# Optimization experiments

Hardware: AMD Instinct MI355X
Metric: run time of the kernel (lower is better)

## Reference

```python
import jax, jax.numpy as jnp
import numpy as np

H = 16  # num_heads


def _rotate_half(t):
    d = t.shape[-1] // 2
    return jnp.concatenate((-t[..., d:], t[..., :d]), axis=-1)


def setup_inputs() -> dict:
    key = jax.random.key(0)
    ks = jax.random.split(key, 4)
    S, HID = 2048, 1280
    D = HID // H  # 80
    x = jax.random.normal(ks[0], (S, HID), dtype=jnp.float32)
    # rotary tables (seq_len, head_dim)
    inv_freq = 1.0 / (10000.0 ** (jnp.arange(0, D, 2, dtype=jnp.float32) / D))
    freqs = jnp.arange(S, dtype=jnp.float32)[:, None] * inv_freq[None, :]  # (S, D/2)
    emb = jnp.concatenate([freqs, freqs], axis=-1)  # (S, D)
    cos = jnp.cos(emb)
    sin = jnp.sin(emb)
    W_qkv = jax.random.normal(ks[1], (HID, 3 * HID), dtype=jnp.float32) * 0.02
    b_qkv = jnp.zeros((3 * HID,), dtype=jnp.float32)
    W_out = jax.random.normal(ks[2], (HID, HID), dtype=jnp.float32) * 0.02
    b_out = jnp.zeros((HID,), dtype=jnp.float32)
    # 8 windows of 256 tokens each -> block-diagonal attention
    cu_seqlens = jnp.arange(0, S + 1, 256, dtype=jnp.int32)  # (9,)
    return {"x": x, "cos": cos, "sin": sin, "W_qkv": W_qkv, "b_qkv": b_qkv,
            "W_out": W_out, "b_out": b_out, "cu_seqlens": cu_seqlens}


def _segment_mask(cu_seqlens, seq_len, dtype):
    positions = jnp.arange(seq_len)
    starts = cu_seqlens[:-1]
    ends = cu_seqlens[1:]
    in_segment = (positions[:, None] >= starts[None, :]) & (positions[:, None] < ends[None, :])
    segment_ids = jnp.argmax(in_segment.astype(jnp.int32), axis=-1)  # (S,)
    same_segment = segment_ids[:, None] == segment_ids[None, :]      # (S, S)
    return jnp.where(same_segment, jnp.zeros((), dtype), jnp.finfo(dtype).min)


def reference(x, cos, sin, W_qkv, b_qkv, W_out, b_out, cu_seqlens):
    S, HID = x.shape
    D = HID // H
    scale = D ** -0.5
    qkv = x @ W_qkv + b_qkv                       # (S, 3*HID)
    q, k, v = jnp.split(qkv, 3, axis=-1)
    q = q.reshape(S, H, D)
    k = k.reshape(S, H, D)
    v = v.reshape(S, H, D)
    cos_f = cos[:, :D][:, None, :]                # (S, 1, D)
    sin_f = sin[:, :D][:, None, :]
    q = q * cos_f + _rotate_half(q) * sin_f       # inline RoPE (fp32)
    k = k * cos_f + _rotate_half(k) * sin_f
    q = jnp.transpose(q, (1, 0, 2))               # (H, S, D)
    k = jnp.transpose(k, (1, 0, 2))
    v = jnp.transpose(v, (1, 0, 2))
    scores = jnp.einsum('hqd,hkd->hqk', q, k) * scale  # (H, S, S)
    mask = _segment_mask(cu_seqlens, S, scores.dtype)  # (S, S) block-diagonal bias
    scores = scores + mask[None, :, :]
    weights = jax.nn.softmax(scores, axis=-1)
    out = jnp.einsum('hqk,hkd->hqd', weights, v)       # (H, S, D)
    out = jnp.transpose(out, (1, 0, 2)).reshape(S, HID)
    return out @ W_out + b_out
```

## Files before the change

kernel.cpp:

```cpp
#include <hip/hip_runtime.h>


typedef short s16x8 __attribute__((ext_vector_type(8)));
typedef __bf16 bf16x8 __attribute__((ext_vector_type(8)));
typedef float f32x4 __attribute__((ext_vector_type(4)));
typedef unsigned short u16;
typedef unsigned long long u64;

__device__ __forceinline__ f32x4 mfma16(s16x8 a, s16x8 b, f32x4 c) {
  return __builtin_amdgcn_mfma_f32_16x16x32_bf16(
      __builtin_bit_cast(bf16x8, a), __builtin_bit_cast(bf16x8, b), c, 0, 0, 0);
}
__device__ __forceinline__ u16 f2b(float f) {
  union { float f; unsigned u; } v;
  v.f = f;
  unsigned r = v.u + 0x7fffu + ((v.u >> 16) & 1u);
  return (u16)(r >> 16);
}
__device__ __forceinline__ void gl16(const u16* g, u16* l) {
  __builtin_amdgcn_global_load_lds(
      (const __attribute__((address_space(1))) unsigned int*)(const void*)g,
      (__attribute__((address_space(3))) unsigned int*)(void*)l, 16, 0, 0);
}

__device__ __forceinline__ void transpose_body(const float* __restrict__ W,
                                               u16* __restrict__ WT, int K, int N,
                                               int nb, int kb, int t, float (*tile)[33]) {
  int tx = t & 31, ty = t >> 5;
#pragma unroll
  for (int r = 0; r < 32; r += 8)
    tile[ty + r][tx] = W[(long)(kb + ty + r) * N + nb + tx];
  __syncthreads();
#pragma unroll
  for (int r = 0; r < 32; r += 8)
    WT[(long)(nb + ty + r) * K + kb + tx] = f2b(tile[tx][ty + r]);
}

__global__ __launch_bounds__(256) void prep(const float* __restrict__ x,
                                            u16* __restrict__ xb,
                                            const float* __restrict__ Wqkv,
                                            u16* __restrict__ WqkvT,
                                            const float* __restrict__ Wout,
                                            u16* __restrict__ WoutT) {
  __shared__ float tile[32][33];
  int bid = blockIdx.x, t = threadIdx.x;
  if (bid < 2560) {
    int i = bid * 256 + t;
    float4 v = ((const float4*)x)[i];
    u64 pk = (u64)f2b(v.x) | ((u64)f2b(v.y) << 16) | ((u64)f2b(v.z) << 32) |
             ((u64)f2b(v.w) << 48);
    ((u64*)xb)[i] = pk;
  } else if (bid < 7360) {
    int i = bid - 2560;
    transpose_body(Wqkv, WqkvT, 1280, 3840, (i % 120) * 32, (i / 120) * 32, t, tile);
  } else {
    int i = bid - 7360;
    transpose_body(Wout, WoutT, 1280, 1280, (i % 40) * 32, (i / 40) * 32, t, tile);
  }
}

__global__ __launch_bounds__(512, 4) void gemm_qkv_rope(const u16* __restrict__ A,
                                                        const u16* __restrict__ B,
                                                        const float* __restrict__ bias,
                                                        const float* __restrict__ cosb,
                                                        const float* __restrict__ sinb,
                                                        u16* __restrict__ Qr,
                                                        u16* __restrict__ Kr,
                                                        u16* __restrict__ VT) {
  __shared__ u16 As[2][128 * 64];
  __shared__ u16 Bs[2][160 * 64];
  const int K = 1280;
  int i = blockIdx.x;
  int xcd = i & 7, j = i >> 3;
  int n0 = (xcd * 3 + (j % 3)) * 160;
  int m0 = (j / 3) * 128;
  int t = threadIdx.x, w = t >> 6, lane = t & 63, lm = lane & 15, quad = lane >> 4;
  int wm = (w >> 1) * 32, wn = (w & 1) * 80;

  const u16* AgSrc[2];
  const u16* BgSrc[3];
#pragma unroll
  for (int c = 0; c < 2; c++) {
    int g = c * 512 + t, row = g >> 3, chp = g & 7;
    AgSrc[c] = A + (long)(m0 + row) * K + ((chp ^ (row & 7)) << 3);
  }
#pragma unroll
  for (int c = 0; c < 2; c++) {
    int g = c * 512 + t, row = g >> 3, chp = g & 7;
    BgSrc[c] = B + (long)(n0 + row) * K + ((chp ^ (row & 7)) << 3);
  }
  {
    int g = 1024 + t, row = g >> 3, chp = g & 7;
    BgSrc[2] = B + (long)(n0 + row) * K + ((chp ^ (row & 7)) << 3);
  }

  auto stage = [&](int buf, int k0) {
#pragma unroll
    for (int c = 0; c < 2; c++) gl16(AgSrc[c] + k0, &As[buf][c * 4096 + w * 512]);
#pragma unroll
    for (int c = 0; c < 2; c++) gl16(BgSrc[c] + k0, &Bs[buf][c * 4096 + w * 512]);
    if (t < 256) gl16(BgSrc[2] + k0, &Bs[buf][8192 + w * 512]);
  };

  f32x4 acc[2][5] = {};
  stage(0, 0);
  int buf = 0;
  for (int k0 = 0; k0 < K; k0 += 64) {
    __syncthreads();
    if (k0 + 64 < K) stage(buf ^ 1, k0 + 64);
#pragma unroll
    for (int kh = 0; kh < 2; kh++) {
      s16x8 af[2], bfr[5];
#pragma unroll
      for (int mt = 0; mt < 2; mt++) {
        int rm = wm + mt * 16 + lm;
        af[mt] = *(const s16x8*)&As[buf][rm * 64 + (((kh * 4 + quad) ^ (rm & 7)) << 3)];
      }
#pragma unroll
      for (int nt = 0; nt < 5; nt++) {
        int rn = wn + nt * 16 + lm;
        bfr[nt] = *(const s16x8*)&Bs[buf][rn * 64 + (((kh * 4 + quad) ^ (rn & 7)) << 3)];
      }
#pragma unroll
      for (int mt = 0; mt < 2; mt++)
#pragma unroll
        for (int nt = 0; nt < 5; nt++)
          acc[mt][nt] = mfma16(af[mt], bfr[nt], acc[mt][nt]);
    }
    buf ^= 1;
  }

  int region = n0 / 1280;
  int hcol = (n0 - region * 1280 + wn) / 80;
  float bv[5];
#pragma unroll
  for (int nt = 0; nt < 5; nt++) bv[nt] = bias[n0 + wn + nt * 16 + lm];

  if (region == 2) {
#pragma unroll
    for (int mt = 0; mt < 2; mt++) {
      int sbase = m0 + wm + mt * 16 + quad * 4;
#pragma unroll
      for (int nt = 0; nt < 5; nt++) {
        int d = nt * 16 + lm;
        u64 pk = 0;
#pragma unroll
        for (int r = 0; r < 4; r++)
          pk |= (u64)f2b(acc[mt][nt][r] + bv[nt]) << (16 * r);
        *(u64*)&VT[((long)hcol * 80 + d) * 2048 + sbase] = pk;
      }
    }
    return;
  }

  const float scale = 0.111803398874989f;
  bool lo = lm < 8;
  u16* Out = (region == 0) ? Qr : Kr;
  float oscale = (region == 0) ? scale : 1.0f;
#pragma unroll
  for (int mt = 0; mt < 2; mt++)
#pragma unroll
    for (int r = 0; r < 4; r++) {
      int s = m0 + wm + mt * 16 + quad * 4 + r;
      float val[5], sw[5];
#pragma unroll
      for (int nt = 0; nt < 5; nt++) val[nt] = acc[mt][nt][r] + bv[nt];
#pragma unroll
      for (int nt = 0; nt < 5; nt++) sw[nt] = __shfl_xor(val[nt], 8);
      float rot[5];
      rot[0] = -(lo ? sw[2] : sw[3]);
      rot[1] = -(lo ? sw[3] : sw[4]);
      rot[2] = lo ? -sw[4] : sw[0];
      rot[3] = lo ? sw[0] : sw[1];
      rot[4] = lo ? sw[1] : sw[2];
      u16* orow = Out + ((long)hcol * 2048 + s) * 80;
      const float* crow = cosb + s * 80;
      const float* srw = sinb + s * 80;
#pragma unroll
      for (int nt = 0; nt < 5; nt++) {
        int d = nt * 16 + lm;
        orow[d] = f2b((val[nt] * crow[d] + rot[nt] * srw[d]) * oscale);
      }
    }
}

__global__ __launch_bounds__(512, 2) void gemm_out(const u16* __restrict__ A,
                                                   const u16* __restrict__ B,
                                                   const float* __restrict__ bias,
                                                   float* __restrict__ C) {
  __shared__ u16 As[2][64 * 64];
  __shared__ u16 Bs[2][160 * 64];
  const int K = 1280;
  int i = blockIdx.x;
  int xcd = i & 7, m0 = (i >> 3) * 64, n0 = xcd * 160;
  int t = threadIdx.x, w = t >> 6, lane = t & 63, lm = lane & 15, quad = lane >> 4;
  int wm = (w >> 1) * 16, wn = (w & 1) * 80;

  const u16* AgSrc;
  {
    int row = t >> 3, chp = t & 7;
    AgSrc = A + (long)(m0 + row) * K + ((chp ^ (row & 7)) << 3);
  }
  const u16* BgSrc[3];
#pragma unroll
  for (int c = 0; c < 2; c++) {
    int g = c * 512 + t, row = g >> 3, chp = g & 7;
    BgSrc[c] = B + (long)(n0 + row) * K + ((chp ^ (row & 7)) << 3);
  }
  {
    int g = 1024 + t, row = g >> 3, chp = g & 7;
    BgSrc[2] = B + (long)(n0 + row) * K + ((chp ^ (row & 7)) << 3);
  }

  auto stage = [&](int buf, int k0) {
    gl16(AgSrc + k0, &As[buf][w * 512]);
#pragma unroll
    for (int c = 0; c < 2; c++) gl16(BgSrc[c] + k0, &Bs[buf][c * 4096 + w * 512]);
    if (t < 256) gl16(BgSrc[2] + k0, &Bs[buf][8192 + w * 512]);
  };

  f32x4 acc[5] = {};
  stage(0, 0);
  int buf = 0;
  for (int k0 = 0; k0 < K; k0 += 64) {
    __syncthreads();
    if (k0 + 64 < K) stage(buf ^ 1, k0 + 64);
#pragma unroll
    for (int kh = 0; kh < 2; kh++) {
      int rm = wm + lm;
      s16x8 af = *(const s16x8*)&As[buf][rm * 64 + (((kh * 4 + quad) ^ (rm & 7)) << 3)];
      s16x8 bfr[5];
#pragma unroll
      for (int nt = 0; nt < 5; nt++) {
        int rn = wn + nt * 16 + lm;
        bfr[nt] = *(const s16x8*)&Bs[buf][rn * 64 + (((kh * 4 + quad) ^ (rn & 7)) << 3)];
      }
#pragma unroll
      for (int nt = 0; nt < 5; nt++) acc[nt] = mfma16(af, bfr[nt], acc[nt]);
    }
    buf ^= 1;
  }
#pragma unroll
  for (int nt = 0; nt < 5; nt++) {
    int col = n0 + wn + nt * 16 + lm;
    float bvv = bias[col];
#pragma unroll
    for (int r = 0; r < 4; r++) {
      int row = m0 + wm + quad * 4 + r;
      C[(long)row * 1280 + col] = acc[nt][r] + bvv;
    }
  }
}

__global__ __launch_bounds__(256, 2) void attn_kernel(const u16* __restrict__ Qr,
                                                      const u16* __restrict__ Kr,
                                                      const u16* __restrict__ VT,
                                                      u16* __restrict__ AO) {
  int qb = blockIdx.x, seg = blockIdx.y, h = blockIdx.z;
  int t = threadIdx.x;
  int w = t >> 6, lane = t & 63, lm = lane & 15, quad = lane >> 4;
  __shared__ u16 Ps[4][16 * 256];

  int s0 = seg * 256 + qb * 64 + w * 16;
  const u16* Qh = Qr + ((long)h * 2048 + s0) * 80;
  const u16* Kh = Kr + ((long)h * 2048 + seg * 256) * 80;

  f32x4 sc[16] = {};
  s16x8 zz = {};
#pragma unroll
  for (int kk = 0; kk < 3; kk++) {
    int dbase = kk * 32 + quad * 8;
    bool valid = dbase < 80;
    s16x8 af = valid ? *(const s16x8*)(Qh + lm * 80 + dbase) : zz;
#pragma unroll
    for (int nt = 0; nt < 16; nt++) {
      s16x8 bfr = valid ? *(const s16x8*)(Kh + (nt * 16 + lm) * 80 + dbase) : zz;
      sc[nt] = mfma16(af, bfr, sc[nt]);
    }
  }

  float rowinv[4];
#pragma unroll
  for (int r = 0; r < 4; r++) {
    float m = sc[0][r];
#pragma unroll
    for (int nt = 1; nt < 16; nt++) m = fmaxf(m, sc[nt][r]);
    m = fmaxf(m, __shfl_xor(m, 1));
    m = fmaxf(m, __shfl_xor(m, 2));
    m = fmaxf(m, __shfl_xor(m, 4));
    m = fmaxf(m, __shfl_xor(m, 8));
    float s = 0.f;
#pragma unroll
    for (int nt = 0; nt < 16; nt++) {
      float e = __expf(sc[nt][r] - m);
      sc[nt][r] = e;
      s += e;
    }
    s += __shfl_xor(s, 1);
    s += __shfl_xor(s, 2);
    s += __shfl_xor(s, 4);
    s += __shfl_xor(s, 8);
    rowinv[r] = 1.0f / s;
    int row = quad * 4 + r;
#pragma unroll
    for (int nt = 0; nt < 16; nt++) {
      int chunk = nt * 2 + (lm >> 3);
      Ps[w][row * 256 + ((chunk ^ row) << 3) + (lm & 7)] = f2b(sc[nt][r]);
    }
  }
  asm volatile("s_waitcnt lgkmcnt(0)" ::: "memory");

  f32x4 oacc[5] = {};
  const u16* Vh = VT + (long)h * 80 * 2048 + seg * 256;
#pragma unroll
  for (int kc = 0; kc < 8; kc++) {
    int row = lm;
    s16x8 pa = *(const s16x8*)&Ps[w][row * 256 + (((kc * 4 + quad) ^ row) << 3)];
#pragma unroll
    for (int nt = 0; nt < 5; nt++) {
      s16x8 bvv = *(const s16x8*)(Vh + (long)(nt * 16 + lm) * 2048 + kc * 32 + quad * 8);
      oacc[nt] = mfma16(pa, bvv, oacc[nt]);
    }
  }
#pragma unroll
  for (int nt = 0; nt < 5; nt++)
#pragma unroll
    for (int r = 0; r < 4; r++)
      AO[(long)(s0 + quad * 4 + r) * 1280 + h * 80 + nt * 16 + lm] =
          f2b(oacc[nt][r] * rowinv[r]);
}

extern "C" void kernel_launch(void* const* d_in, const int* in_sizes, int n_in,
                              void* d_out, int out_size, void* d_ws, size_t ws_size,
                              hipStream_t stream) {
  const float* x    = (const float*)d_in[0];
  const float* cosb = (const float*)d_in[1];
  const float* sinb = (const float*)d_in[2];
  const float* Wqkv = (const float*)d_in[3];
  const float* bqkv = (const float*)d_in[4];
  const float* Wout = (const float*)d_in[5];
  const float* bout = (const float*)d_in[6];

  char* p = (char*)d_ws;
  u16* xb    = (u16*)p;
  u16* WqkvT = (u16*)(p + 5242880);
  u16* WoutT = (u16*)(p + 15073280);
  u16* Qr    = (u16*)(p + 18350080);
  u16* Kr    = (u16*)(p + 23592960);
  u16* VT    = (u16*)(p + 28835840);
  u16* AO    = xb;

  prep<<<dim3(8960), dim3(256), 0, stream>>>(x, xb, Wqkv, WqkvT, Wout, WoutT);
  gemm_qkv_rope<<<dim3(384), dim3(512), 0, stream>>>(xb, WqkvT, bqkv, cosb, sinb,
                                                     Qr, Kr, VT);
  attn_kernel<<<dim3(4, 8, 16), dim3(256), 0, stream>>>(Qr, Kr, VT, AO);
  gemm_out<<<dim3(256), dim3(512), 0, stream>>>(AO, WoutT, bout, (float*)d_out);
}
```

Baseline: 161.8 us.

## Fuse prep, QKV GEMM, attention and output GEMM into one cooperative persistent kernel

```diff
diff --git a/kernel.cpp b/kernel.cpp
--- a/kernel.cpp
+++ b/kernel.cpp
@@ -23,6 +23,19 @@
       (__attribute__((address_space(3))) unsigned int*)(void*)l, 16, 0, 0);
 }
 
+__device__ __forceinline__ void grid_barrier(unsigned* bar, unsigned target) {
+  __threadfence();
+  __syncthreads();
+  if (threadIdx.x == 0) {
+    __hip_atomic_fetch_add(bar, 1u, __ATOMIC_RELEASE, __HIP_MEMORY_SCOPE_AGENT);
+    while (__hip_atomic_load(bar, __ATOMIC_ACQUIRE, __HIP_MEMORY_SCOPE_AGENT) <
+           target)
+      __builtin_amdgcn_s_sleep(8);
+  }
+  __syncthreads();
+  __threadfence();
+}
+
 __device__ __forceinline__ void transpose_body(const float* __restrict__ W,
                                                u16* __restrict__ WT, int K, int N,
                                                int nb, int kb, int t, float (*tile)[33]) {
@@ -36,189 +49,273 @@
     WT[(long)(nb + ty + r) * K + kb + tx] = f2b(tile[tx][ty + r]);
 }
 
-__global__ __launch_bounds__(256) void prep(const float* __restrict__ x,
-                                            u16* __restrict__ xb,
-                                            const float* __restrict__ Wqkv,
-                                            u16* __restrict__ WqkvT,
-                                            const float* __restrict__ Wout,
-                                            u16* __restrict__ WoutT) {
-  __shared__ float tile[32][33];
-  int bid = blockIdx.x, t = threadIdx.x;
-  if (bid < 2560) {
-    int i = bid * 256 + t;
-    float4 v = ((const float4*)x)[i];
-    u64 pk = (u64)f2b(v.x) | ((u64)f2b(v.y) << 16) | ((u64)f2b(v.z) << 32) |
-             ((u64)f2b(v.w) << 48);
-    ((u64*)xb)[i] = pk;
-  } else if (bid < 7360) {
-    int i = bid - 2560;
-    transpose_body(Wqkv, WqkvT, 1280, 3840, (i % 120) * 32, (i / 120) * 32, t, tile);
-  } else {
-    int i = bid - 7360;
-    transpose_body(Wout, WoutT, 1280, 1280, (i % 40) * 32, (i / 40) * 32, t, tile);
-  }
-}
-
-__global__ __launch_bounds__(512, 4) void gemm_qkv_rope(const u16* __restrict__ A,
-                                                        const u16* __restrict__ B,
-                                                        const float* __restrict__ bias,
-                                                        const float* __restrict__ cosb,
-                                                        const float* __restrict__ sinb,
-                                                        u16* __restrict__ Qr,
-                                                        u16* __restrict__ Kr,
-                                                        u16* __restrict__ VT) {
-  __shared__ u16 As[2][128 * 64];
-  __shared__ u16 Bs[2][160 * 64];
+__device__ __forceinline__ void prep_phase(int bid, int stride, int t, char* pool,
+                                           const float* __restrict__ x,
+                                           u16* __restrict__ xb,
+                                           const float* __restrict__ Wqkv,
+                                           u16* __restrict__ WqkvT,
+                                           const float* __restrict__ Wout,
+                                           u16* __restrict__ WoutT) {
+  float (*tile)[33] = (float(*)[33])pool;
+  for (int u = bid; u < 8960; u += stride) {
+    if (u < 2560) {
+      int i = u * 256 + t;
+      float4 v = ((const float4*)x)[i];
+      u64 pk = (u64)f2b(v.x) | ((u64)f2b(v.y) << 16) | ((u64)f2b(v.z) << 32) |
+               ((u64)f2b(v.w) << 48);
+      ((u64*)xb)[i] = pk;
+    } else if (u < 7360) {
+      int i = u - 2560;
+      transpose_body(Wqkv, WqkvT, 1280, 3840, (i % 120) * 32, (i / 120) * 32, t, tile);
+      __syncthreads();
+    } else {
+      int i = u - 7360;
+      transpose_body(Wout, WoutT, 1280, 1280, (i % 40) * 32, (i / 40) * 32, t, tile);
+      __syncthreads();
+    }
+  }
+}
+
+__device__ __forceinline__ void gemm1_phase(int bid, int stride, int t, char* pool,
+                                            const u16* __restrict__ A,
+                                            const u16* __restrict__ B,
+                                            const float* __restrict__ bias,
+                                            const float* __restrict__ cosb,
+                                            const float* __restrict__ sinb,
+                                            u16* __restrict__ Qr,
+                                            u16* __restrict__ Kr,
+                                            u16* __restrict__ VT) {
+  u16* As = (u16*)pool;
+  u16* Bs = (u16*)(pool + 16384);
   const int K = 1280;
-  int i = blockIdx.x;
-  int xcd = i & 7, j = i >> 3;
-  int n0 = (xcd * 3 + (j % 3)) * 160;
-  int m0 = (j / 3) * 128;
-  int t = threadIdx.x, w = t >> 6, lane = t & 63, lm = lane & 15, quad = lane >> 4;
+  int w = t >> 6, lane = t & 63, lm = lane & 15, quad = lane >> 4;
   int wm = (w >> 1) * 32, wn = (w & 1) * 80;
+  for (int u = bid; u < 768; u += stride) {
+    int xcd = u & 7, j = u >> 3;
+    int n0 = (xcd * 3 + (j % 3)) * 160;
+    int m0 = (j / 3) * 64;
+    const u16* AgSrc[2];
+    const u16* BgSrc[5];
+#pragma unroll
+    for (int c = 0; c < 2; c++) {
+      int g = c * 256 + t, row = g >> 3, chp = g & 7;
+      AgSrc[c] = A + (long)(m0 + row) * K + ((chp ^ (row & 7)) << 3);
+    }
+#pragma unroll
+    for (int c = 0; c < 5; c++) {
+      int g = c * 256 + t, row = g >> 3, chp = g & 7;
+      BgSrc[c] = B + (long)(n0 + row) * K + ((chp ^ (row & 7)) << 3);
+    }
+    auto stage = [&](int buf, int k0) {
+#pragma unroll
+      for (int c = 0; c < 2; c++)
+        gl16(AgSrc[c] + k0, As + buf * 4096 + c * 2048 + w * 512);
+#pragma unroll
+      for (int c = 0; c < 5; c++)
+        gl16(BgSrc[c] + k0, Bs + buf * 10240 + c * 2048 + w * 512);
+    };
+    f32x4 acc[2][5] = {};
+    stage(0, 0);
+    int buf = 0;
+    for (int k0 = 0; k0 < K; k0 += 64) {
+      __syncthreads();
+      if (k0 + 64 < K) stage(buf ^ 1, k0 + 64);
+#pragma unroll
+      for (int kh = 0; kh < 2; kh++) {
+        s16x8 af[2], bfr[5];
+#pragma unroll
+        for (int mt = 0; mt < 2; mt++) {
+          int rm = wm + mt * 16 + lm;
+          af[mt] = *(const s16x8*)&As[buf * 4096 + rm * 64 +
+                                      (((kh * 4 + quad) ^ (rm & 7)) << 3)];
+        }
+#pragma unroll
+        for (int nt = 0; nt < 5; nt++) {
+          int rn = wn + nt * 16 + lm;
+          bfr[nt] = *(const s16x8*)&Bs[buf * 10240 + rn * 64 +
+                                       (((kh * 4 + quad) ^ (rn & 7)) << 3)];
+        }
+#pragma unroll
+        for (int mt = 0; mt < 2; mt++)
+#pragma unroll
+          for (int nt = 0; nt < 5; nt++)
+            acc[mt][nt] = mfma16(af[mt], bfr[nt], acc[mt][nt]);
+      }
+      buf ^= 1;
+    }
+    __syncthreads();
+
+    int region = n0 / 1280;
+    int hcol = (n0 - region * 1280 + wn) / 80;
+    float bv[5];
+#pragma unroll
+    for (int nt = 0; nt < 5; nt++) bv[nt] = bias[n0 + wn + nt * 16 + lm];
+
+    if (region == 2) {
+#pragma unroll
+      for (int mt = 0; mt < 2; mt++) {
+        int sbase = m0 + wm + mt * 16 + quad * 4;
+#pragma unroll
+        for (int nt = 0; nt < 5; nt++) {
+          int d = nt * 16 + lm;
+          u64 pk = 0;
+#pragma unroll
+          for (int r = 0; r < 4; r++)
+            pk |= (u64)f2b(acc[mt][nt][r] + bv[nt]) << (16 * r);
+          *(u64*)&VT[((long)hcol * 80 + d) * 2048 + sbase] = pk;
+        }
+      }
+      continue;
+    }
+
+    const float scale = 0.111803398874989f;
+    bool lo = lm < 8;
+    u16* Out = (region == 0) ? Qr : Kr;
+    float oscale = (region == 0) ? scale : 1.0f;
+#pragma unroll
+    for (int mt = 0; mt < 2; mt++)
+#pragma unroll
+      for (int r = 0; r < 4; r++) {
+        int s = m0 + wm + mt * 16 + quad * 4 + r;
+        float val[5], sw[5];
+#pragma unroll
+        for (int nt = 0; nt < 5; nt++) val[nt] = acc[mt][nt][r] + bv[nt];
+#pragma unroll
+        for (int nt = 0; nt < 5; nt++) sw[nt] = __shfl_xor(val[nt], 8);
+        float rot[5];
+        rot[0] = -(lo ? sw[2] : sw[3]);
+        rot[1] = -(lo ? sw[3] : sw[4]);
+        rot[2] = lo ? -sw[4] : sw[0];
+        rot[3] = lo ? sw[0] : sw[1];
+        rot[4] = lo ? sw[1] : sw[2];
+        u16* orow = Out + ((long)hcol * 2048 + s) * 80;
+        const float* crow = cosb + s * 80;
+        const float* srw = sinb + s * 80;
+#pragma unroll
+        for (int nt = 0; nt < 5; nt++) {
+          int d = nt * 16 + lm;
+          orow[d] = f2b((val[nt] * crow[d] + rot[nt] * srw[d]) * oscale);
+        }
+      }
+  }
+}
+
+__device__ __forceinline__ void attn_phase(int bid, int t, char* pool,
+                                           const u16* __restrict__ Qr,
+                                           const u16* __restrict__ Kr,
+                                           const u16* __restrict__ VT,
+                                           u16* __restrict__ AO) {
+  u16* Ps = (u16*)pool;
+  int w = t >> 6, lane = t & 63, lm = lane & 15, quad = lane >> 4;
+  int qb = bid & 3, seg = (bid >> 2) & 7, h = bid >> 5;
+
+  int s0 = seg * 256 + qb * 64 + w * 16;
+  const u16* Qh = Qr + ((long)h * 2048 + s0) * 80;
+  const u16* Kh = Kr + ((long)h * 2048 + seg * 256) * 80;
+
+  f32x4 sc[16] = {};
+  s16x8 zz = {};
+#pragma unroll
+  for (int kk = 0; kk < 3; kk++) {
+    int dbase = kk * 32 + quad * 8;
+    bool valid = dbase < 80;
+    s16x8 af = valid ? *(const s16x8*)(Qh + lm * 80 + dbase) : zz;
+#pragma unroll
+    for (int nt = 0; nt < 16; nt++) {
+      s16x8 bfr = valid ? *(const s16x8*)(Kh + (nt * 16 + lm) * 80 + dbase) : zz;
+      sc[nt] = mfma16(af, bfr, sc[nt]);
+    }
+  }
+
+  float rowinv[4];
+#pragma unroll
+  for (int r = 0; r < 4; r++) {
+    float m = sc[0][r];
+#pragma unroll
+    for (int nt = 1; nt < 16; nt++) m = fmaxf(m, sc[nt][r]);
+    m = fmaxf(m, __shfl_xor(m, 1));
+    m = fmaxf(m, __shfl_xor(m, 2));
+    m = fmaxf(m, __shfl_xor(m, 4));
+    m = fmaxf(m, __shfl_xor(m, 8));
+    float s = 0.f;
+#pragma unroll
+    for (int nt = 0; nt < 16; nt++) {
+      float e = __expf(sc[nt][r] - m);
+      sc[nt][r] = e;
+      s += e;
+    }
+    s += __shfl_xor(s, 1);
+    s += __shfl_xor(s, 2);
+    s += __shfl_xor(s, 4);
+    s += __shfl_xor(s, 8);
+    rowinv[r] = 1.0f / s;
+    int row = quad * 4 + r;
+#pragma unroll
+    for (int nt = 0; nt < 16; nt++) {
+      int chunk = nt * 2 + (lm >> 3);
+      Ps[w * 4096 + row * 256 + ((chunk ^ row) << 3) + (lm & 7)] = f2b(sc[nt][r]);
+    }
+  }
+  asm volatile("s_waitcnt lgkmcnt(0)" ::: "memory");
+
+  f32x4 oacc[5] = {};
+  const u16* Vh = VT + (long)h * 80 * 2048 + seg * 256;
+#pragma unroll
+  for (int kc = 0; kc < 8; kc++) {
+    int row = lm;
+    s16x8 pa = *(const s16x8*)&Ps[w * 4096 + row * 256 + (((kc * 4 + quad) ^ row) << 3)];
+#pragma unroll
+    for (int nt = 0; nt < 5; nt++) {
+      s16x8 bvv = *(const s16x8*)(Vh + (long)(nt * 16 + lm) * 2048 + kc * 32 + quad * 8);
+      oacc[nt] = mfma16(pa, bvv, oacc[nt]);
+    }
+  }
+#pragma unroll
+  for (int nt = 0; nt < 5; nt++)
+#pragma unroll
+    for (int r = 0; r < 4; r++)
+      AO[(long)(s0 + quad * 4 + r) * 1280 + h * 80 + nt * 16 + lm] =
+          f2b(oacc[nt][r] * rowinv[r]);
+}
+
+__device__ __forceinline__ void gemm2_phase(int bid, int t, char* pool,
+                                            const u16* __restrict__ A,
+                                            const u16* __restrict__ B,
+                                            const float* __restrict__ bias,
+                                            float* __restrict__ C) {
+  u16* As = (u16*)pool;
+  u16* Bs = (u16*)(pool + 16384);
+  const int K = 1280;
+  int w = t >> 6, lane = t & 63, lm = lane & 15, quad = lane >> 4;
+  int wm = w * 16;
+  int n0 = (bid & 7) * 160 + ((bid >> 3) & 1) * 80;
+  int m0 = (bid >> 4) * 64;
 
   const u16* AgSrc[2];
+#pragma unroll
+  for (int c = 0; c < 2; c++) {
+    int g = c * 256 + t, row = g >> 3, chp = g & 7;
+    AgSrc[c] = A + (long)(m0 + row) * K + ((chp ^ (row & 7)) << 3);
+  }
   const u16* BgSrc[3];
 #pragma unroll
   for (int c = 0; c < 2; c++) {
-    int g = c * 512 + t, row = g >> 3, chp = g & 7;
-    AgSrc[c] = A + (long)(m0 + row) * K + ((chp ^ (row & 7)) << 3);
-  }
-#pragma unroll
-  for (int c = 0; c < 2; c++) {
-    int g = c * 512 + t, row = g >> 3, chp = g & 7;
+    int g = c * 256 + t, row = g >> 3, chp = g & 7;
     BgSrc[c] = B + (long)(n0 + row) * K + ((chp ^ (row & 7)) << 3);
   }
   {
-    int g = 1024 + t, row = g >> 3, chp = g & 7;
+    int g = 512 + t, row = g >> 3, chp = g & 7;
     BgSrc[2] = B + (long)(n0 + row) * K + ((chp ^ (row & 7)) << 3);
   }
-
   auto stage = [&](int buf, int k0) {
 #pragma unroll
-    for (int c = 0; c < 2; c++) gl16(AgSrc[c] + k0, &As[buf][c * 4096 + w * 512]);
-#pragma unroll
-    for (int c = 0; c < 2; c++) gl16(BgSrc[c] + k0, &Bs[buf][c * 4096 + w * 512]);
-    if (t < 256) gl16(BgSrc[2] + k0, &Bs[buf][8192 + w * 512]);
+    for (int c = 0; c < 2; c++)
+      gl16(AgSrc[c] + k0, As + buf * 4096 + c * 2048 + w * 512);
+#pragma unroll
+    for (int c = 0; c < 2; c++)
+      gl16(BgSrc[c] + k0, Bs + buf * 5120 + c * 2048 + w * 512);
+    if (t < 128) gl16(BgSrc[2] + k0, Bs + buf * 5120 + 4096 + w * 512);
   };
-
-  f32x4 acc[2][5] = {};
-  stage(0, 0);
-  int buf = 0;
-  for (int k0 = 0; k0 < K; k0 += 64) {
-    __syncthreads();
-    if (k0 + 64 < K) stage(buf ^ 1, k0 + 64);
-#pragma unroll
-    for (int kh = 0; kh < 2; kh++) {
-      s16x8 af[2], bfr[5];
-#pragma unroll
-      for (int mt = 0; mt < 2; mt++) {
-        int rm = wm + mt * 16 + lm;
-        af[mt] = *(const s16x8*)&As[buf][rm * 64 + (((kh * 4 + quad) ^ (rm & 7)) << 3)];
-      }
-#pragma unroll
-      for (int nt = 0; nt < 5; nt++) {
-        int rn = wn + nt * 16 + lm;
-        bfr[nt] = *(const s16x8*)&Bs[buf][rn * 64 + (((kh * 4 + quad) ^ (rn & 7)) << 3)];
-      }
-#pragma unroll
-      for (int mt = 0; mt < 2; mt++)
-#pragma unroll
-        for (int nt = 0; nt < 5; nt++)
-          acc[mt][nt] = mfma16(af[mt], bfr[nt], acc[mt][nt]);
-    }
-    buf ^= 1;
-  }
-
-  int region = n0 / 1280;
-  int hcol = (n0 - region * 1280 + wn) / 80;
-  float bv[5];
-#pragma unroll
-  for (int nt = 0; nt < 5; nt++) bv[nt] = bias[n0 + wn + nt * 16 + lm];
-
-  if (region == 2) {
-#pragma unroll
-    for (int mt = 0; mt < 2; mt++) {
-      int sbase = m0 + wm + mt * 16 + quad * 4;
-#pragma unroll
-      for (int nt = 0; nt < 5; nt++) {
-        int d = nt * 16 + lm;
-        u64 pk = 0;
-#pragma unroll
-        for (int r = 0; r < 4; r++)
-          pk |= (u64)f2b(acc[mt][nt][r] + bv[nt]) << (16 * r);
-        *(u64*)&VT[((long)hcol * 80 + d) * 2048 + sbase] = pk;
-      }
-    }
-    return;
-  }
-
-  const float scale = 0.111803398874989f;
-  bool lo = lm < 8;
-  u16* Out = (region == 0) ? Qr : Kr;
-  float oscale = (region == 0) ? scale : 1.0f;
-#pragma unroll
-  for (int mt = 0; mt < 2; mt++)
-#pragma unroll
-    for (int r = 0; r < 4; r++) {
-      int s = m0 + wm + mt * 16 + quad * 4 + r;
-      float val[5], sw[5];
-#pragma unroll
-      for (int nt = 0; nt < 5; nt++) val[nt] = acc[mt][nt][r] + bv[nt];
-#pragma unroll
-      for (int nt = 0; nt < 5; nt++) sw[nt] = __shfl_xor(val[nt], 8);
-      float rot[5];
-      rot[0] = -(lo ? sw[2] : sw[3]);
-      rot[1] = -(lo ? sw[3] : sw[4]);
-      rot[2] = lo ? -sw[4] : sw[0];
-      rot[3] = lo ? sw[0] : sw[1];
-      rot[4] = lo ? sw[1] : sw[2];
-      u16* orow = Out + ((long)hcol * 2048 + s) * 80;
-      const float* crow = cosb + s * 80;
-      const float* srw = sinb + s * 80;
-#pragma unroll
-      for (int nt = 0; nt < 5; nt++) {
-        int d = nt * 16 + lm;
-        orow[d] = f2b((val[nt] * crow[d] + rot[nt] * srw[d]) * oscale);
-      }
-    }
-}
-
-__global__ __launch_bounds__(512, 2) void gemm_out(const u16* __restrict__ A,
-                                                   const u16* __restrict__ B,
-                                                   const float* __restrict__ bias,
-                                                   float* __restrict__ C) {
-  __shared__ u16 As[2][64 * 64];
-  __shared__ u16 Bs[2][160 * 64];
-  const int K = 1280;
-  int i = blockIdx.x;
-  int xcd = i & 7, m0 = (i >> 3) * 64, n0 = xcd * 160;
-  int t = threadIdx.x, w = t >> 6, lane = t & 63, lm = lane & 15, quad = lane >> 4;
-  int wm = (w >> 1) * 16, wn = (w & 1) * 80;
-
-  const u16* AgSrc;
-  {
-    int row = t >> 3, chp = t & 7;
-    AgSrc = A + (long)(m0 + row) * K + ((chp ^ (row & 7)) << 3);
-  }
-  const u16* BgSrc[3];
-#pragma unroll
-  for (int c = 0; c < 2; c++) {
-    int g = c * 512 + t, row = g >> 3, chp = g & 7;
-    BgSrc[c] = B + (long)(n0 + row) * K + ((chp ^ (row & 7)) << 3);
-  }
-  {
-    int g = 1024 + t, row = g >> 3, chp = g & 7;
-    BgSrc[2] = B + (long)(n0 + row) * K + ((chp ^ (row & 7)) << 3);
-  }
-
-  auto stage = [&](int buf, int k0) {
-    gl16(AgSrc + k0, &As[buf][w * 512]);
-#pragma unroll
-    for (int c = 0; c < 2; c++) gl16(BgSrc[c] + k0, &Bs[buf][c * 4096 + w * 512]);
-    if (t < 256) gl16(BgSrc[2] + k0, &Bs[buf][8192 + w * 512]);
-  };
-
   f32x4 acc[5] = {};
   stage(0, 0);
   int buf = 0;
@@ -228,12 +325,14 @@
 #pragma unroll
     for (int kh = 0; kh < 2; kh++) {
       int rm = wm + lm;
-      s16x8 af = *(const s16x8*)&As[buf][rm * 64 + (((kh * 4 + quad) ^ (rm & 7)) << 3)];
+      s16x8 af = *(const s16x8*)&As[buf * 4096 + rm * 64 +
+                                    (((kh * 4 + quad) ^ (rm & 7)) << 3)];
       s16x8 bfr[5];
 #pragma unroll
       for (int nt = 0; nt < 5; nt++) {
-        int rn = wn + nt * 16 + lm;
-        bfr[nt] = *(const s16x8*)&Bs[buf][rn * 64 + (((kh * 4 + quad) ^ (rn & 7)) << 3)];
+        int rn = nt * 16 + lm;
+        bfr[nt] = *(const s16x8*)&Bs[buf * 5120 + rn * 64 +
+                                     (((kh * 4 + quad) ^ (rn & 7)) << 3)];
       }
 #pragma unroll
       for (int nt = 0; nt < 5; nt++) acc[nt] = mfma16(af, bfr[nt], acc[nt]);
@@ -242,7 +341,7 @@
   }
 #pragma unroll
   for (int nt = 0; nt < 5; nt++) {
-    int col = n0 + wn + nt * 16 + lm;
+    int col = n0 + nt * 16 + lm;
     float bvv = bias[col];
 #pragma unroll
     for (int r = 0; r < 4; r++) {
@@ -252,82 +351,61 @@
   }
 }
 
-__global__ __launch_bounds__(256, 2) void attn_kernel(const u16* __restrict__ Qr,
-                                                      const u16* __restrict__ Kr,
-                                                      const u16* __restrict__ VT,
-                                                      u16* __restrict__ AO) {
-  int qb = blockIdx.x, seg = blockIdx.y, h = blockIdx.z;
-  int t = threadIdx.x;
-  int w = t >> 6, lane = t & 63, lm = lane & 15, quad = lane >> 4;
-  __shared__ u16 Ps[4][16 * 256];
-
-  int s0 = seg * 256 + qb * 64 + w * 16;
-  const u16* Qh = Qr + ((long)h * 2048 + s0) * 80;
-  const u16* Kh = Kr + ((long)h * 2048 + seg * 256) * 80;
-
-  f32x4 sc[16] = {};
-  s16x8 zz = {};
-#pragma unroll
-  for (int kk = 0; kk < 3; kk++) {
-    int dbase = kk * 32 + quad * 8;
-    bool valid = dbase < 80;
-    s16x8 af = valid ? *(const s16x8*)(Qh + lm * 80 + dbase) : zz;
-#pragma unroll
-    for (int nt = 0; nt < 16; nt++) {
-      s16x8 bfr = valid ? *(const s16x8*)(Kh + (nt * 16 + lm) * 80 + dbase) : zz;
-      sc[nt] = mfma16(af, bfr, sc[nt]);
-    }
-  }
-
-  float rowinv[4];
-#pragma unroll
-  for (int r = 0; r < 4; r++) {
-    float m = sc[0][r];
-#pragma unroll
-    for (int nt = 1; nt < 16; nt++) m = fmaxf(m, sc[nt][r]);
-    m = fmaxf(m, __shfl_xor(m, 1));
-    m = fmaxf(m, __shfl_xor(m, 2));
-    m = fmaxf(m, __shfl_xor(m, 4));
-    m = fmaxf(m, __shfl_xor(m, 8));
-    float s = 0.f;
-#pragma unroll
-    for (int nt = 0; nt < 16; nt++) {
-      float e = __expf(sc[nt][r] - m);
-      sc[nt][r] = e;
-      s += e;
-    }
-    s += __shfl_xor(s, 1);
-    s += __shfl_xor(s, 2);
-    s += __shfl_xor(s, 4);
-    s += __shfl_xor(s, 8);
-    rowinv[r] = 1.0f / s;
-    int row = quad * 4 + r;
-#pragma unroll
-    for (int nt = 0; nt < 16; nt++) {
-      int chunk = nt * 2 + (lm >> 3);
-      Ps[w][row * 256 + ((chunk ^ row) << 3) + (lm & 7)] = f2b(sc[nt][r]);
-    }
-  }
-  asm volatile("s_waitcnt lgkmcnt(0)" ::: "memory");
-
-  f32x4 oacc[5] = {};
-  const u16* Vh = VT + (long)h * 80 * 2048 + seg * 256;
-#pragma unroll
-  for (int kc = 0; kc < 8; kc++) {
-    int row = lm;
-    s16x8 pa = *(const s16x8*)&Ps[w][row * 256 + (((kc * 4 + quad) ^ row) << 3)];
-#pragma unroll
-    for (int nt = 0; nt < 5; nt++) {
-      s16x8 bvv = *(const s16x8*)(Vh + (long)(nt * 16 + lm) * 2048 + kc * 32 + quad * 8);
-      oacc[nt] = mfma16(pa, bvv, oacc[nt]);
-    }
-  }
-#pragma unroll
-  for (int nt = 0; nt < 5; nt++)
-#pragma unroll
-    for (int r = 0; r < 4; r++)
-      AO[(long)(s0 + quad * 4 + r) * 1280 + h * 80 + nt * 16 + lm] =
-          f2b(oacc[nt][r] * rowinv[r]);
+__global__ __launch_bounds__(256, 2) void fused(
+    const float* __restrict__ x, const float* __restrict__ cosb,
+    const float* __restrict__ sinb, const float* __restrict__ Wqkv,
+    const float* __restrict__ bqkv, const float* __restrict__ Wout,
+    const float* __restrict__ bout, u16* __restrict__ xb,
+    u16* __restrict__ WqkvT, u16* __restrict__ WoutT, u16* __restrict__ Qr,
+    u16* __restrict__ Kr, u16* __restrict__ VT, float* __restrict__ out,
+    unsigned* bar) {
+  __shared__ __attribute__((aligned(16))) char pool[57344];
+  int bid = blockIdx.x, t = threadIdx.x;
+
+  prep_phase(bid, 512, t, pool, x, xb, Wqkv, WqkvT, Wout, WoutT);
+  grid_barrier(bar, 512);
+  gemm1_phase(bid, 512, t, pool, xb, WqkvT, bqkv, cosb, sinb, Qr, Kr, VT);
+  grid_barrier(bar, 1024);
+  attn_phase(bid, t, pool, Qr, Kr, VT, xb);
+  grid_barrier(bar, 1536);
+  gemm2_phase(bid, t, pool, xb, WoutT, bout, out);
+}
+
+__global__ __launch_bounds__(256) void k_prep(const float* __restrict__ x,
+                                              u16* __restrict__ xb,
+                                              const float* __restrict__ Wqkv,
+                                              u16* __restrict__ WqkvT,
+                                              const float* __restrict__ Wout,
+                                              u16* __restrict__ WoutT) {
+  __shared__ __attribute__((aligned(16))) char pool[4224];
+  prep_phase(blockIdx.x, gridDim.x, threadIdx.x, pool, x, xb, Wqkv, WqkvT, Wout,
+             WoutT);
+}
+__global__ __launch_bounds__(256) void k_gemm1(const u16* __restrict__ A,
+                                               const u16* __restrict__ B,
+                                               const float* __restrict__ bias,
+                                               const float* __restrict__ cosb,
+                                               const float* __restrict__ sinb,
+                                               u16* __restrict__ Qr,
+                                               u16* __restrict__ Kr,
+                                               u16* __restrict__ VT) {
+  __shared__ __attribute__((aligned(16))) char pool[57344];
+  gemm1_phase(blockIdx.x, gridDim.x, threadIdx.x, pool, A, B, bias, cosb, sinb,
+              Qr, Kr, VT);
+}
+__global__ __launch_bounds__(256, 2) void k_attn(const u16* __restrict__ Qr,
+                                                 const u16* __restrict__ Kr,
+                                                 const u16* __restrict__ VT,
+                                                 u16* __restrict__ AO) {
+  __shared__ __attribute__((aligned(16))) char pool[32768];
+  attn_phase(blockIdx.x, threadIdx.x, pool, Qr, Kr, VT, AO);
+}
+__global__ __launch_bounds__(256) void k_gemm2(const u16* __restrict__ A,
+                                               const u16* __restrict__ B,
+                                               const float* __restrict__ bias,
+                                               float* __restrict__ C) {
+  __shared__ __attribute__((aligned(16))) char pool[36864];
+  gemm2_phase(blockIdx.x, threadIdx.x, pool, A, B, bias, C);
 }
 
 extern "C" void kernel_launch(void* const* d_in, const int* in_sizes, int n_in,
@@ -348,11 +426,23 @@
   u16* Qr    = (u16*)(p + 18350080);
   u16* Kr    = (u16*)(p + 23592960);
   u16* VT    = (u16*)(p + 28835840);
-  u16* AO    = xb;
-
-  prep<<<dim3(8960), dim3(256), 0, stream>>>(x, xb, Wqkv, WqkvT, Wout, WoutT);
-  gemm_qkv_rope<<<dim3(384), dim3(512), 0, stream>>>(xb, WqkvT, bqkv, cosb, sinb,
-                                                     Qr, Kr, VT);
-  attn_kernel<<<dim3(4, 8, 16), dim3(256), 0, stream>>>(Qr, Kr, VT, AO);
-  gemm_out<<<dim3(256), dim3(512), 0, stream>>>(AO, WoutT, bout, (float*)d_out);
-}
+  float* out = (float*)d_out;
+
+  unsigned* bar = (unsigned*)((char*)d_out + out_size - 4);
+  hipMemsetAsync(bar, 0, 4, stream);
+
+  void* args[] = {(void*)&x,     (void*)&cosb,  (void*)&sinb, (void*)&Wqkv,
+                  (void*)&bqkv,  (void*)&Wout,  (void*)&bout, (void*)&xb,
+                  (void*)&WqkvT, (void*)&WoutT, (void*)&Qr,   (void*)&Kr,
+                  (void*)&VT,    (void*)&out,   (void*)&bar};
+  hipError_t err = hipLaunchCooperativeKernel((void*)fused, dim3(512), dim3(256),
+                                              args, 0, stream);
+  if (err != hipSuccess) {
+    (void)hipGetLastError();
+    k_prep<<<dim3(8960), dim3(256), 0, stream>>>(x, xb, Wqkv, WqkvT, Wout, WoutT);
+    k_gemm1<<<dim3(768), dim3(256), 0, stream>>>(xb, WqkvT, bqkv, cosb, sinb, Qr,
+                                                 Kr, VT);
+    k_attn<<<dim3(512), dim3(256), 0, stream>>>(Qr, Kr, VT, xb);
+    k_gemm2<<<dim3(512), dim3(256), 0, stream>>>(xb, WoutT, bout, out);
+  }
+}
```

After: 613.9 us. +279.5%, slower.

## Use 4-wave single-buffered QKV GEMM with larger per-wave M tile

Applied to the files above, without the earlier changes.

```diff
diff --git a/kernel.cpp b/kernel.cpp
--- a/kernel.cpp
+++ b/kernel.cpp
@@ -59,7 +59,7 @@
   }
 }
 
-__global__ __launch_bounds__(512, 4) void gemm_qkv_rope(const u16* __restrict__ A,
+__global__ __launch_bounds__(256, 4) void gemm_qkv_rope(const u16* __restrict__ A,
                                                         const u16* __restrict__ B,
                                                         const float* __restrict__ bias,
                                                         const float* __restrict__ cosb,
@@ -67,67 +67,54 @@
                                                         u16* __restrict__ Qr,
                                                         u16* __restrict__ Kr,
                                                         u16* __restrict__ VT) {
-  __shared__ u16 As[2][128 * 64];
-  __shared__ u16 Bs[2][160 * 64];
+  __shared__ u16 As[128 * 64];
+  __shared__ u16 Bs[160 * 64];
   const int K = 1280;
   int i = blockIdx.x;
   int xcd = i & 7, j = i >> 3;
   int n0 = (xcd * 3 + (j % 3)) * 160;
   int m0 = (j / 3) * 128;
   int t = threadIdx.x, w = t >> 6, lane = t & 63, lm = lane & 15, quad = lane >> 4;
-  int wm = (w >> 1) * 32, wn = (w & 1) * 80;
-
-  const u16* AgSrc[2];
-  const u16* BgSrc[3];
-#pragma unroll
-  for (int c = 0; c < 2; c++) {
-    int g = c * 512 + t, row = g >> 3, chp = g & 7;
+  int wm = (w >> 1) * 64, wn = (w & 1) * 80;
+
+  const u16* AgSrc[4];
+  const u16* BgSrc[5];
+#pragma unroll
+  for (int c = 0; c < 4; c++) {
+    int g = c * 256 + t, row = g >> 3, chp = g & 7;
     AgSrc[c] = A + (long)(m0 + row) * K + ((chp ^ (row & 7)) << 3);
   }
 #pragma unroll
-  for (int c = 0; c < 2; c++) {
-    int g = c * 512 + t, row = g >> 3, chp = g & 7;
+  for (int c = 0; c < 5; c++) {
+    int g = c * 256 + t, row = g >> 3, chp = g & 7;
     BgSrc[c] = B + (long)(n0 + row) * K + ((chp ^ (row & 7)) << 3);
   }
-  {
-    int g = 1024 + t, row = g >> 3, chp = g & 7;
-    BgSrc[2] = B + (long)(n0 + row) * K + ((chp ^ (row & 7)) << 3);
-  }
-
-  auto stage = [&](int buf, int k0) {
-#pragma unroll
-    for (int c = 0; c < 2; c++) gl16(AgSrc[c] + k0, &As[buf][c * 4096 + w * 512]);
-#pragma unroll
-    for (int c = 0; c < 2; c++) gl16(BgSrc[c] + k0, &Bs[buf][c * 4096 + w * 512]);
-    if (t < 256) gl16(BgSrc[2] + k0, &Bs[buf][8192 + w * 512]);
-  };
-
-  f32x4 acc[2][5] = {};
-  stage(0, 0);
-  int buf = 0;
+
+  f32x4 acc[4][5] = {};
   for (int k0 = 0; k0 < K; k0 += 64) {
     __syncthreads();
-    if (k0 + 64 < K) stage(buf ^ 1, k0 + 64);
+#pragma unroll
+    for (int c = 0; c < 4; c++) gl16(AgSrc[c] + k0, As + c * 2048 + w * 512);
+#pragma unroll
+    for (int c = 0; c < 5; c++) gl16(BgSrc[c] + k0, Bs + c * 2048 + w * 512);
+    __syncthreads();
 #pragma unroll
     for (int kh = 0; kh < 2; kh++) {
-      s16x8 af[2], bfr[5];
-#pragma unroll
-      for (int mt = 0; mt < 2; mt++) {
-        int rm = wm + mt * 16 + lm;
-        af[mt] = *(const s16x8*)&As[buf][rm * 64 + (((kh * 4 + quad) ^ (rm & 7)) << 3)];
-      }
+      s16x8 bfr[5];
 #pragma unroll
       for (int nt = 0; nt < 5; nt++) {
         int rn = wn + nt * 16 + lm;
-        bfr[nt] = *(const s16x8*)&Bs[buf][rn * 64 + (((kh * 4 + quad) ^ (rn & 7)) << 3)];
-      }
-#pragma unroll
-      for (int mt = 0; mt < 2; mt++)
+        bfr[nt] = *(const s16x8*)&Bs[rn * 64 + (((kh * 4 + quad) ^ (rn & 7)) << 3)];
+      }
+#pragma unroll
+      for (int mt = 0; mt < 4; mt++) {
+        int rm = wm + mt * 16 + lm;
+        s16x8 af = *(const s16x8*)&As[rm * 64 + (((kh * 4 + quad) ^ (rm & 7)) << 3)];
 #pragma unroll
         for (int nt = 0; nt < 5; nt++)
-          acc[mt][nt] = mfma16(af[mt], bfr[nt], acc[mt][nt]);
-    }
-    buf ^= 1;
+          acc[mt][nt] = mfma16(af, bfr[nt], acc[mt][nt]);
+      }
+    }
   }
 
   int region = n0 / 1280;
@@ -138,7 +125,7 @@
 
   if (region == 2) {
 #pragma unroll
-    for (int mt = 0; mt < 2; mt++) {
+    for (int mt = 0; mt < 4; mt++) {
       int sbase = m0 + wm + mt * 16 + quad * 4;
 #pragma unroll
       for (int nt = 0; nt < 5; nt++) {
@@ -158,7 +145,7 @@
   u16* Out = (region == 0) ? Qr : Kr;
   float oscale = (region == 0) ? scale : 1.0f;
 #pragma unroll
-  for (int mt = 0; mt < 2; mt++)
+  for (int mt = 0; mt < 4; mt++)
 #pragma unroll
     for (int r = 0; r < 4; r++) {
       int s = m0 + wm + mt * 16 + quad * 4 + r;
@@ -351,7 +338,7 @@
   u16* AO    = xb;
 
   prep<<<dim3(8960), dim3(256), 0, stream>>>(x, xb, Wqkv, WqkvT, Wout, WoutT);
-  gemm_qkv_rope<<<dim3(384), dim3(512), 0, stream>>>(xb, WqkvT, bqkv, cosb, sinb,
+  gemm_qkv_rope<<<dim3(384), dim3(256), 0, stream>>>(xb, WqkvT, bqkv, cosb, sinb,
                                                      Qr, Kr, VT);
   attn_kernel<<<dim3(4, 8, 16), dim3(256), 0, stream>>>(Qr, Kr, VT, AO);
   gemm_out<<<dim3(256), dim3(512), 0, stream>>>(AO, WoutT, bout, (float*)d_out);
```

Result: slower. 171.1 us (+5.8%).
